# Kernel tuning notes

Hardware: AMD Instinct MI355X
Metric: run time of the kernel (lower is better)

Reference implementation:

```python
import jax, jax.numpy as jnp
import numpy as np

B, S, P, G, E = 16, 1024, 32, 64, 512
HD = E // 2          # head_dim = 256
SCALE = HD ** -0.5
LAMBDA_INIT = 0.8 - 0.6 * float(np.exp(-0.3 * 0.0))  # depth=0 -> 0.2
EPS = 1e-5


def setup_inputs() -> dict:
    key = jax.random.key(0)
    ks = jax.random.split(key, 12)
    inp = {
        'query': jax.random.normal(ks[0], (B, S, E), jnp.float32),
        'key': jax.random.normal(ks[1], (B, P, G, E), jnp.float32),
        'mask': jax.random.randint(ks[2], (B, S), 0, 2).astype(bool),
        'Wq': jax.random.normal(ks[3], (E, E), jnp.float32) * (E ** -0.5),
        'Wk': jax.random.normal(ks[4], (E, E), jnp.float32) * (E ** -0.5),
        'Wv': jax.random.normal(ks[5], (E, E), jnp.float32) * (E ** -0.5),
        'Wo': jax.random.normal(ks[6], (E, E), jnp.float32) * (E ** -0.5),
        'lq1': jax.random.normal(ks[7], (HD,), jnp.float32) * 0.1,
        'lk1': jax.random.normal(ks[8], (HD,), jnp.float32) * 0.1,
        'lq2': jax.random.normal(ks[9], (HD,), jnp.float32) * 0.1,
        'lk2': jax.random.normal(ks[10], (HD,), jnp.float32) * 0.1,
        'gamma': jnp.ones((E,), jnp.float32),
    }
    return inp


def reference(query, key, mask, Wq, Wk, Wv, Wo, lq1, lk1, lq2, lk2, gamma):
    b, s, e = query.shape
    _, p, g, _ = key.shape
    L = p * g
    key2d = key.reshape(b, L, e)

    Q = (query @ Wq).reshape(b, s, 2, HD).transpose(0, 2, 1, 3) * SCALE  # [B,2,S,hd]
    K = (key2d @ Wk).reshape(b, L, 2, HD).transpose(0, 2, 1, 3)          # [B,2,L,hd]
    V = key2d @ Wv                                                       # [B,L,E]

    scores = jnp.einsum('bhsd,bhld->bhsl', Q, K)                         # [B,2,S,L]
    # masked_fill(~mask, 0.0) with mask broadcast [B,1,S,1]
    scores = jnp.where(mask[:, None, :, None], scores, 0.0)
    attn = jax.nn.softmax(scores, axis=-1)

    lam1 = jnp.exp(jnp.sum(lq1 * lk1))
    lam2 = jnp.exp(jnp.sum(lq2 * lk2))
    lam = lam1 - lam2 + LAMBDA_INIT

    diff = attn[:, 0] - lam * attn[:, 1]                                 # [B,S,L]
    out2d = jnp.einsum('bsl,ble->bse', diff, V)                          # [B,S,E]

    # RMSNorm over last dim with affine gamma
    rms = out2d * jax.lax.rsqrt(jnp.mean(out2d * out2d, axis=-1, keepdims=True) + EPS)
    rms = rms * gamma
    out = (rms * (1.0 - LAMBDA_INIT)) @ Wo                               # [B,S,E]

    return out, diff.reshape(b, s, p, g)
```

## Files before the change

kernel.cpp:

```cpp
#include <hip/hip_runtime.h>
#include <hip/hip_bf16.h>


typedef short short8 __attribute__((ext_vector_type(8)));
typedef __bf16 bf16x8 __attribute__((ext_vector_type(8)));
typedef float f32x4 __attribute__((ext_vector_type(4)));

#define LDS_BYTES 16384
#define OUT0_ELEMS 8388608L

__global__ void probe_kernel(const void* gamma, const void* mask, int* flags)
{
    if (threadIdx.x == 0) {
        unsigned g = *(const unsigned*)gamma;
        flags[0] = (g == 0x3F800000u) ? 1 : 0;
        flags[1] = 0;
    }
    __syncthreads();
    const unsigned* mi = (const unsigned*)mask;
    int bad = 0;
    for (int i = threadIdx.x; i < 4096; i += blockDim.x)
        if (mi[i] > 1u) bad = 1;
    if (bad) atomicOr(&flags[1], 1);
}

__global__ void convert_mask(const void* __restrict__ mask, int* __restrict__ mi,
                             const int* __restrict__ flags)
{
    int i = blockIdx.x * 256 + threadIdx.x;
    if (flags[1]) mi[i] = ((const unsigned char*)mask)[i] ? 1 : 0;
    else          mi[i] = ((const int*)mask)[i] ? 1 : 0;
}

__device__ __forceinline__ float read_elem(const void* p, int i, int isf32)
{
    return isf32 ? ((const float*)p)[i]
                 : __bfloat162float(((const __hip_bfloat16*)p)[i]);
}

__global__ void convert_gamma(const void* __restrict__ gamma, float* __restrict__ g,
                              const int* __restrict__ flags)
{
    int i = blockIdx.x * 256 + threadIdx.x;
    g[i] = read_elem(gamma, i, flags[0]);
}

__global__ void transpose_w(const void* __restrict__ Wq, const void* __restrict__ Wk,
                            const void* __restrict__ Wv, const void* __restrict__ Wo,
                            __hip_bfloat16* __restrict__ dst, const int* __restrict__ flags)
{
    int which = blockIdx.y;
    const void* s = (which == 0) ? Wq : (which == 1) ? Wk : (which == 2) ? Wv : Wo;
    __hip_bfloat16* d = dst + (long)which * 262144;
    int idx = blockIdx.x * 256 + threadIdx.x;
    int k = idx >> 9, n = idx & 511;
    d[n * 512 + k] = __float2bfloat16(read_elem(s, idx, flags[0]));
}

__global__ void lam_kernel(const void* __restrict__ lq1, const void* __restrict__ lk1,
                           const void* __restrict__ lq2, const void* __restrict__ lk2,
                           float* __restrict__ lamp, const int* __restrict__ flags)
{
    int t = threadIdx.x;
    int f = flags[0];
    float s1 = 0.0f, s2 = 0.0f;
#pragma unroll
    for (int j = 0; j < 4; ++j) {
        int idx = t * 4 + j;
        s1 += read_elem(lq1, idx, f) * read_elem(lk1, idx, f);
        s2 += read_elem(lq2, idx, f) * read_elem(lk2, idx, f);
    }
#pragma unroll
    for (int off = 1; off < 64; off <<= 1) {
        s1 += __shfl_xor(s1, off);
        s2 += __shfl_xor(s2, off);
    }
    if (t == 0) *lamp = __expf(s1) - __expf(s2) + 0.2f;
}

__global__ void zero_lst(float* __restrict__ lst)
{
    lst[blockIdx.x * 256 + threadIdx.x] = 0.0f;
}

__device__ __forceinline__ void stage_u(const void* A, long aoff, int lda, int af32,
                                        const __hip_bfloat16* B, int ldb,
                                        int kt, char* smem, int tid)
{
    if (af32) {
#pragma unroll
        for (int j = 0; j < 2; ++j) {
            int chunk = j * 256 + tid;
            const float* g = (const float*)A + aoff + (long)(chunk >> 2) * lda + kt + (chunk & 3) * 8;
            f32x4 x0 = *(const f32x4*)g;
            f32x4 x1 = *(const f32x4*)(g + 4);
            __hip_bfloat16 tmp[8];
#pragma unroll
            for (int t = 0; t < 4; ++t) tmp[t] = __float2bfloat16(x0[t]);
#pragma unroll
            for (int t = 0; t < 4; ++t) tmp[4 + t] = __float2bfloat16(x1[t]);
            *(short8*)(smem + chunk * 16) = *(const short8*)tmp;
        }
    } else {
#pragma unroll
        for (int j = 0; j < 2; ++j) {
            int chunk = j * 256 + tid;
            const __hip_bfloat16* g = (const __hip_bfloat16*)A + aoff
                                    + (long)(chunk >> 2) * lda + kt + (chunk & 3) * 8;
            __builtin_amdgcn_global_load_lds(
                (__attribute__((address_space(1))) void*)g,
                (__attribute__((address_space(3))) void*)(smem + chunk * 16), 16, 0, 0);
        }
    }
#pragma unroll
    for (int j = 0; j < 2; ++j) {
        int chunk = j * 256 + tid;
        const __hip_bfloat16* g = B + (long)(chunk >> 2) * ldb + kt + (chunk & 3) * 8;
        __builtin_amdgcn_global_load_lds(
            (__attribute__((address_space(1))) void*)g,
            (__attribute__((address_space(3))) void*)(smem + 8192 + chunk * 16), 16, 0, 0);
    }
}

__device__ __forceinline__ void mfma_block(char* smem, int tid, f32x4 (&acc)[4][4])
{
    const int lane = tid & 63, wid = tid >> 6;
    const int wm = wid >> 1, wn = wid & 1;
    const int lm = lane & 15, lq = lane >> 4;
    short8 a[4], b[4];
#pragma unroll
    for (int i = 0; i < 4; ++i)
        a[i] = *(const short8*)(smem + (wm * 64 + i * 16 + lm) * 64 + lq * 16);
#pragma unroll
    for (int i = 0; i < 4; ++i)
        b[i] = *(const short8*)(smem + 8192 + (wn * 64 + i * 16 + lm) * 64 + lq * 16);
#pragma unroll
    for (int i = 0; i < 4; ++i)
#pragma unroll
        for (int j = 0; j < 4; ++j)
            acc[i][j] = __builtin_amdgcn_mfma_f32_16x16x32_bf16(
                __builtin_bit_cast(bf16x8, a[i]),
                __builtin_bit_cast(bf16x8, b[j]),
                acc[i][j], 0, 0, 0);
}

__device__ __forceinline__ void zero_acc(f32x4 (&acc)[4][4])
{
#pragma unroll
    for (int i = 0; i < 4; ++i)
#pragma unroll
        for (int j = 0; j < 4; ++j)
#pragma unroll
            for (int r = 0; r < 4; ++r) acc[i][j][r] = 0.0f;
}

__device__ __forceinline__ void tile_gemm_u(const void* A, long aoff, int lda, int af32,
                                            const __hip_bfloat16* B, int ldb, int K,
                                            char* smem, int tid, f32x4 (&acc)[4][4])
{
    zero_acc(acc);
    for (int kt = 0; kt < K; kt += 32) {
        __syncthreads();
        stage_u(A, aoff, lda, af32, B, ldb, kt, smem, tid);
        __syncthreads();
        mfma_block(smem, tid, acc);
    }
}

template <int MODE, int AF>
__launch_bounds__(256, 4)
__global__ void gemm_u(const void* __restrict__ A,
                       const __hip_bfloat16* __restrict__ B,
                       void* __restrict__ C,
                       int K, int lda, int ldb, int ldc,
                       long sA, long sB, long sC, float scale,
                       const int* __restrict__ flags)
{
    __shared__ __align__(16) char smem[LDS_BYTES];
    const int tid = threadIdx.x;
    const int bn = blockIdx.x, bm = blockIdx.y, bz = blockIdx.z;
    const int af32 = AF ? flags[0] : 0;
    const long aoff = (long)bz * sA + (long)bm * 128 * lda;
    const __hip_bfloat16* Bb = B + (long)bz * sB + (long)bn * 128 * ldb;

    f32x4 acc[4][4];
    tile_gemm_u(A, aoff, lda, af32, Bb, ldb, K, smem, tid, acc);

    const int f32o = (MODE == 3) ? flags[0] : 0;
    const int lane = tid & 63, wid = tid >> 6;
    const int wm = wid >> 1, wn = wid & 1;
    const int lm = lane & 15, lq = lane >> 4;
#pragma unroll
    for (int im = 0; im < 4; ++im)
#pragma unroll
        for (int in = 0; in < 4; ++in)
#pragma unroll
            for (int r = 0; r < 4; ++r) {
                int row = bm * 128 + wm * 64 + im * 16 + lq * 4 + r;
                int col = bn * 128 + wn * 64 + in * 16 + lm;
                float v = acc[im][in][r] * scale;
                if (MODE == 0) {
                    ((__hip_bfloat16*)C)[bz * sC + (long)row * ldc + col] = __float2bfloat16(v);
                } else if (MODE == 2) {
                    ((float*)C)[bz * sC + (long)row * ldc + col] = v;
                } else if (MODE == 3) {
                    long idx = bz * sC + (long)row * ldc + col;
                    if (f32o) ((float*)C)[idx] = v;
                    else      ((__hip_bfloat16*)C)[idx] = __float2bfloat16(v);
                } else {
                    int bb = row >> 11, l = row & 2047;
                    ((__hip_bfloat16*)C)[((long)bb * 512 + col) * 2048 + l] = __float2bfloat16(v);
                }
            }
}

__device__ __forceinline__ void score_epilogue(
    f32x4 (&acc)[4][4], char* smem, int tid,
    int nt, int st, int b, int bl, const int* __restrict__ mask,
    float* __restrict__ lstats, __hip_bfloat16* __restrict__ P, int h)
{
    const int lane = tid & 63, wid = tid >> 6;
    const int wm = wid >> 1, wn = wid & 1;
    const int lm = lane & 15, lq = lane >> 4;
    float esum[4][4];
#pragma unroll
    for (int im = 0; im < 4; ++im)
#pragma unroll
        for (int r = 0; r < 4; ++r) {
            int rl = wm * 64 + im * 16 + lq * 4 + r;
            int s  = st * 128 + rl;
            int mv = mask[b * 1024 + s];
            float es = 0.0f;
#pragma unroll
            for (int in = 0; in < 4; ++in) {
                int col = nt * 128 + wn * 64 + in * 16 + lm;
                float sc = mv ? acc[im][in][r] : 0.0f;
                float e  = __expf(sc);
                P[((long)bl * 1024 + s) * 2048 + col] = __float2bfloat16(e);
                float t = e;
                t += __shfl_xor(t, 1);
                t += __shfl_xor(t, 2);
                t += __shfl_xor(t, 4);
                t += __shfl_xor(t, 8);
                es += t;
            }
            esum[im][r] = es;
        }
    __syncthreads();
    float* red = (float*)smem;
    if (lm == 0) {
#pragma unroll
        for (int im = 0; im < 4; ++im)
#pragma unroll
            for (int r = 0; r < 4; ++r)
                red[wn * 128 + wm * 64 + im * 16 + lq * 4 + r] = esum[im][r];
    }
    __syncthreads();
    if (tid < 128)
        atomicAdd(&lstats[((long)(b * 2 + h)) * 1024 + st * 128 + tid],
                  red[tid] + red[128 + tid]);
}

__launch_bounds__(256, 3)
__global__ void score_kernel(const __hip_bfloat16* __restrict__ Q,
                             const __hip_bfloat16* __restrict__ Km,
                             const int* __restrict__ mask,
                             float* __restrict__ lstats,
                             __hip_bfloat16* __restrict__ P0,
                             __hip_bfloat16* __restrict__ P1,
                             int bbase)
{
    __shared__ __align__(16) char smem[LDS_BYTES];
    const int tid = threadIdx.x;
    const int nt = blockIdx.x, st = blockIdx.y, bl = blockIdx.z;
    const int b = bl + bbase;
    const long A0 = ((long)b * 1024 + st * 128) * 512;
    const __hip_bfloat16* B0 = Km + ((long)b * 2048 + nt * 128) * 512;

    f32x4 acc[4][4];
    tile_gemm_u(Q, A0, 512, 0, B0, 512, 256, smem, tid, acc);
    score_epilogue(acc, smem, tid, nt, st, b, bl, mask, lstats, P0, 0);
    tile_gemm_u(Q, A0 + 256, 512, 0, B0 + 256, 512, 256, smem, tid, acc);
    score_epilogue(acc, smem, tid, nt, st, b, bl, mask, lstats, P1, 1);
}

__global__ void finalize_kernel(__hip_bfloat16* P0,
                                const __hip_bfloat16* __restrict__ P1,
                                const float* __restrict__ lstats,
                                const float* __restrict__ lamp,
                                void* dout, int bbase,
                                const int* __restrict__ flags)
{
    const long row = blockIdx.x;
    const int bl = (int)(row >> 10), s = (int)(row & 1023);
    const int b  = bl + bbase;
    const int tid = threadIdx.x;
    const float lam = *lamp;
    const float i0 = 1.0f / lstats[((long)(b * 2)) * 1024 + s];
    const float i1 = lam  / lstats[((long)(b * 2 + 1)) * 1024 + s];
    const long lbase = row * 2048 + (long)tid * 8;

    union { short8 v; __hip_bfloat16 h[8]; } u0, u1, ub;
    u0.v = *(const short8*)(P0 + lbase);
    u1.v = *(const short8*)(P1 + lbase);
    float d[8];
#pragma unroll
    for (int j = 0; j < 8; ++j)
        d[j] = __bfloat162float(u0.h[j]) * i0 - __bfloat162float(u1.h[j]) * i1;

    const long gidx = ((long)b * 1024 + s) * 2048 + (long)tid * 8;
    if (flags[0]) {
        float* outF = (float*)dout + OUT0_ELEMS;
        f32x4 v0, v1;
#pragma unroll
        for (int j = 0; j < 4; ++j) { v0[j] = d[j]; v1[j] = d[4 + j]; }
        *(f32x4*)(outF + gidx)     = v0;
        *(f32x4*)(outF + gidx + 4) = v1;
    } else {
        __hip_bfloat16* outH = (__hip_bfloat16*)dout + OUT0_ELEMS;
        union { short8 v; __hip_bfloat16 h[8]; } uo;
#pragma unroll
        for (int j = 0; j < 8; ++j) uo.h[j] = __float2bfloat16(d[j]);
        *(short8*)(outH + gidx) = uo.v;
    }
#pragma unroll
    for (int j = 0; j < 8; ++j) ub.h[j] = __float2bfloat16(d[j]);
    *(short8*)(P0 + lbase) = ub.v;
}

__global__ void rmsnorm_kernel(const float* __restrict__ X,
                               const float* __restrict__ gamma,
                               __hip_bfloat16* __restrict__ Y)
{
    long row = blockIdx.x;
    int lane = threadIdx.x;
    const float* x = X + row * 512 + lane * 8;
    f32x4 v0 = *(const f32x4*)x;
    f32x4 v1 = *(const f32x4*)(x + 4);
    float ss = v0[0] * v0[0] + v0[1] * v0[1] + v0[2] * v0[2] + v0[3] * v0[3]
             + v1[0] * v1[0] + v1[1] * v1[1] + v1[2] * v1[2] + v1[3] * v1[3];
#pragma unroll
    for (int off = 1; off < 64; off <<= 1) ss += __shfl_xor(ss, off);
    float rinv = rsqrtf(ss * (1.0f / 512.0f) + 1e-5f) * 0.8f;
#pragma unroll
    for (int j = 0; j < 4; ++j)
        Y[row * 512 + lane * 8 + j] = __float2bfloat16(v0[j] * rinv * gamma[lane * 8 + j]);
#pragma unroll
    for (int j = 0; j < 4; ++j)
        Y[row * 512 + lane * 8 + 4 + j] = __float2bfloat16(v1[j] * rinv * gamma[lane * 8 + 4 + j]);
}

extern "C" void kernel_launch(void* const* d_in, const int* in_sizes, int n_in,
                              void* d_out, int out_size, void* d_ws, size_t ws_size,
                              hipStream_t stream)
{
    const void* query = d_in[0];
    const void* key2d = d_in[1];
    const void* maskp = d_in[2];
    const void* Wq    = d_in[3];
    const void* Wk    = d_in[4];
    const void* Wv    = d_in[5];
    const void* Wo    = d_in[6];
    const void* lq1   = d_in[7];
    const void* lk1   = d_in[8];
    const void* lq2   = d_in[9];
    const void* lk2   = d_in[10];
    const void* gamma = d_in[11];

    char* w = (char*)d_ws;
    __hip_bfloat16* WT    = (__hip_bfloat16*)(w);
    __hip_bfloat16* WqT   = WT;
    __hip_bfloat16* WkT   = WT + 262144;
    __hip_bfloat16* WvT   = WT + 524288;
    __hip_bfloat16* WoT   = WT + 786432;
    float*          lamp  = (float*)(w + 2097152);
    int*            flags = (int*)(w + 2097216);
    float*          gammaF= (float*)(w + 2097280);
    int*            maskI = (int*)(w + 2162688);
    __hip_bfloat16* Qb    = (__hip_bfloat16*)(w + 2228224);
    __hip_bfloat16* Kb    = (__hip_bfloat16*)(w + 19005440);
    __hip_bfloat16* Vt    = (__hip_bfloat16*)(w + 52559872);
    float*          lst   = (float*)(w + 86114304);
    float*          o2d   = (float*)(w + 86245376);
    __hip_bfloat16* rmsb  = (__hip_bfloat16*)(w + 119799808);
    __hip_bfloat16* diffBF= (__hip_bfloat16*)(w + 136577024);
    __hip_bfloat16* P1s   = (__hip_bfloat16*)(w + 103022592);

    const bool bigws = ws_size >= (136577024UL + 67108864UL);

    probe_kernel<<<1, 256, 0, stream>>>(gamma, maskp, flags);
    convert_mask<<<64, 256, 0, stream>>>(maskp, maskI, flags);
    convert_gamma<<<2, 256, 0, stream>>>(gamma, gammaF, flags);
    transpose_w<<<dim3(1024, 4, 1), 256, 0, stream>>>(Wq, Wk, Wv, Wo, WT, flags);
    lam_kernel<<<1, 64, 0, stream>>>(lq1, lk1, lq2, lk2, lamp, flags);
    zero_lst<<<128, 256, 0, stream>>>(lst);

    gemm_u<0, 1><<<dim3(4, 128, 1), 256, 0, stream>>>(query, WqT, Qb,
        512, 512, 512, 512, 0, 0, 0, 0.0625f, flags);
    gemm_u<0, 1><<<dim3(4, 256, 1), 256, 0, stream>>>(key2d, WkT, Kb,
        512, 512, 512, 512, 0, 0, 0, 1.0f, flags);
    gemm_u<1, 1><<<dim3(4, 256, 1), 256, 0, stream>>>(key2d, WvT, Vt,
        512, 512, 512, 0, 0, 0, 0, 1.0f, flags);

    if (bigws) {
        for (int h = 0; h < 2; ++h) {
            int bb = h * 8;
            __hip_bfloat16* P0 = diffBF + (long)bb * 1024 * 2048;
            score_kernel<<<dim3(16, 8, 8), 256, 0, stream>>>(Qb, Kb, maskI, lst,
                P0, P1s, bb);
            finalize_kernel<<<8192, 256, 0, stream>>>(P0, P1s, lst, lamp,
                d_out, bb, flags);
        }
        gemm_u<2, 0><<<dim3(4, 8, 16), 256, 0, stream>>>(diffBF, Vt, o2d,
            2048, 2048, 2048, 512, 1024L * 2048, 512L * 2048, 1024L * 512, 1.0f, flags);
    } else {
        __hip_bfloat16* scratch = (__hip_bfloat16*)d_out;
        for (int h = 0; h < 2; ++h) {
            int bb = h * 8;
            score_kernel<<<dim3(16, 8, 8), 256, 0, stream>>>(Qb, Kb, maskI, lst,
                scratch, P1s, bb);
            finalize_kernel<<<8192, 256, 0, stream>>>(scratch, P1s, lst, lamp,
                d_out, bb, flags);
            gemm_u<2, 0><<<dim3(4, 8, 8), 256, 0, stream>>>(scratch,
                Vt + (long)bb * 512 * 2048, o2d + (long)bb * 1024 * 512,
                2048, 2048, 2048, 512, 1024L * 2048, 512L * 2048, 1024L * 512, 1.0f, flags);
        }
    }

    rmsnorm_kernel<<<16384, 64, 0, stream>>>(o2d, gammaF, rmsb);

    gemm_u<3, 0><<<dim3(4, 128, 1), 256, 0, stream>>>(rmsb, WoT, d_out,
        512, 512, 512, 512, 0, 0, 1024L * 512, 1.0f, flags);
}
```

Measured before the change: 646.0 us.

## Fuse softmax normalization and diff computation into the diff@V GEMM

Adds a dv_fused kernel that reads the unnormalized score probabilities P0/P1, applies the per-row softmax normalizers and lambda to form diff on the fly, stages it in LDS, and runs the MFMA GEMM against V. The blocks with bn==0 also write diff to the output. This removes the separate finalize kernel and the write and re-read of the diff matrix. With a large enough workspace, all 16 batches are also handled in a single score launch. In exchange, the A operand is now loaded synchronously with conversion arithmetic and no async prefetch, and P0/P1 are read four times, once per column block.

After: 672.1 us. +4.0%, slower.

```diff
diff --git a/kernel.cpp b/kernel.cpp
--- a/kernel.cpp
+++ b/kernel.cpp
@@ -282,6 +282,97 @@
     score_epilogue(acc, smem, tid, nt, st, b, bl, mask, lstats, P0, 0);
     tile_gemm_u(Q, A0 + 256, 512, 0, B0 + 256, 512, 256, smem, tid, acc);
     score_epilogue(acc, smem, tid, nt, st, b, bl, mask, lstats, P1, 1);
+}
+
+__launch_bounds__(256, 3)
+__global__ void dv_fused(const __hip_bfloat16* __restrict__ P0,
+                         const __hip_bfloat16* __restrict__ P1,
+                         const __hip_bfloat16* __restrict__ Vt,
+                         const float* __restrict__ lst,
+                         const float* __restrict__ lamp,
+                         float* __restrict__ o2d,
+                         void* __restrict__ dout,
+                         int bbase, const int* __restrict__ flags)
+{
+    __shared__ __align__(16) char smem[LDS_BYTES];
+    const int tid = threadIdx.x;
+    const int bn = blockIdx.x, bm = blockIdx.y, bz = blockIdx.z;
+    const int b = bz + bbase;
+    const float lam = *lamp;
+
+    int srow[2]; float i0[2], i1[2];
+#pragma unroll
+    for (int j = 0; j < 2; ++j) {
+        srow[j] = bm * 128 + j * 64 + (tid >> 2);
+        i0[j] = 1.0f / lst[((long)(b * 2)) * 1024 + srow[j]];
+        i1[j] = lam  / lst[((long)(b * 2 + 1)) * 1024 + srow[j]];
+    }
+
+    const __hip_bfloat16* Bb = Vt + (long)b * (512L * 2048) + (long)bn * 128 * 2048;
+    const int f32o = flags[0];
+    float* doutF = (float*)dout + OUT0_ELEMS;
+    __hip_bfloat16* doutH = (__hip_bfloat16*)dout + OUT0_ELEMS;
+
+    f32x4 acc[4][4];
+    zero_acc(acc);
+
+    for (int kt = 0; kt < 2048; kt += 32) {
+        __syncthreads();
+#pragma unroll
+        for (int j = 0; j < 2; ++j) {
+            int chunk = j * 256 + tid;
+            int kc = kt + (chunk & 3) * 8;
+            long off = ((long)bz * 1024 + srow[j]) * 2048 + kc;
+            union { short8 v; __hip_bfloat16 h[8]; } u0, u1;
+            u0.v = *(const short8*)(P0 + off);
+            u1.v = *(const short8*)(P1 + off);
+            float d[8];
+#pragma unroll
+            for (int t = 0; t < 8; ++t)
+                d[t] = __bfloat162float(u0.h[t]) * i0[j]
+                     - __bfloat162float(u1.h[t]) * i1[j];
+            __hip_bfloat16 tmp[8];
+#pragma unroll
+            for (int t = 0; t < 8; ++t) tmp[t] = __float2bfloat16(d[t]);
+            *(short8*)(smem + chunk * 16) = *(const short8*)tmp;
+            if (bn == 0) {
+                long g = ((long)b * 1024 + srow[j]) * 2048 + kc;
+                if (f32o) {
+                    f32x4 v0, v1;
+#pragma unroll
+                    for (int t = 0; t < 4; ++t) { v0[t] = d[t]; v1[t] = d[4 + t]; }
+                    *(f32x4*)(doutF + g)     = v0;
+                    *(f32x4*)(doutF + g + 4) = v1;
+                } else {
+                    *(short8*)(doutH + g) = *(const short8*)tmp;
+                }
+            }
+        }
+#pragma unroll
+        for (int j = 0; j < 2; ++j) {
+            int chunk = j * 256 + tid;
+            const __hip_bfloat16* g = Bb + (long)(chunk >> 2) * 2048 + kt + (chunk & 3) * 8;
+            __builtin_amdgcn_global_load_lds(
+                (__attribute__((address_space(1))) void*)g,
+                (__attribute__((address_space(3))) void*)(smem + 8192 + chunk * 16), 16, 0, 0);
+        }
+        __syncthreads();
+        mfma_block(smem, tid, acc);
+    }
+
+    const int lane = tid & 63, wid = tid >> 6;
+    const int wm = wid >> 1, wn = wid & 1;
+    const int lm = lane & 15, lq = lane >> 4;
+#pragma unroll
+    for (int im = 0; im < 4; ++im)
+#pragma unroll
+        for (int in = 0; in < 4; ++in)
+#pragma unroll
+            for (int r = 0; r < 4; ++r) {
+                int row = bm * 128 + wm * 64 + im * 16 + lq * 4 + r;
+                int col = bn * 128 + wn * 64 + in * 16 + lm;
+                o2d[((long)b * 1024 + row) * 512 + col] = acc[im][in][r];
+            }
 }
 
 __global__ void finalize_kernel(__hip_bfloat16* P0,
@@ -386,7 +477,8 @@
     __hip_bfloat16* diffBF= (__hip_bfloat16*)(w + 136577024);
     __hip_bfloat16* P1s   = (__hip_bfloat16*)(w + 103022592);
 
-    const bool bigws = ws_size >= (136577024UL + 67108864UL);
+    const bool hugews = ws_size >= 270794752UL;
+    const bool bigws  = ws_size >= 203685888UL;
 
     probe_kernel<<<1, 256, 0, stream>>>(gamma, maskp, flags);
     convert_mask<<<64, 256, 0, stream>>>(maskp, maskI, flags);
@@ -402,17 +494,23 @@
     gemm_u<1, 1><<<dim3(4, 256, 1), 256, 0, stream>>>(key2d, WvT, Vt,
         512, 512, 512, 0, 0, 0, 0, 1.0f, flags);
 
-    if (bigws) {
+    if (hugews) {
+        __hip_bfloat16* P0f = diffBF;
+        __hip_bfloat16* P1f = diffBF + 33554432L;
+        score_kernel<<<dim3(16, 8, 16), 256, 0, stream>>>(Qb, Kb, maskI, lst,
+            P0f, P1f, 0);
+        dv_fused<<<dim3(4, 8, 16), 256, 0, stream>>>(P0f, P1f, Vt, lst, lamp,
+            o2d, d_out, 0, flags);
+    } else if (bigws) {
+        __hip_bfloat16* P0h = diffBF;
+        __hip_bfloat16* P1h = diffBF + 16777216L;
         for (int h = 0; h < 2; ++h) {
             int bb = h * 8;
-            __hip_bfloat16* P0 = diffBF + (long)bb * 1024 * 2048;
             score_kernel<<<dim3(16, 8, 8), 256, 0, stream>>>(Qb, Kb, maskI, lst,
-                P0, P1s, bb);
-            finalize_kernel<<<8192, 256, 0, stream>>>(P0, P1s, lst, lamp,
-                d_out, bb, flags);
-        }
-        gemm_u<2, 0><<<dim3(4, 8, 16), 256, 0, stream>>>(diffBF, Vt, o2d,
-            2048, 2048, 2048, 512, 1024L * 2048, 512L * 2048, 1024L * 512, 1.0f, flags);
+                P0h, P1h, bb);
+            dv_fused<<<dim3(4, 8, 8), 256, 0, stream>>>(P0h, P1h, Vt, lst, lamp,
+                o2d, d_out, bb, flags);
+        }
     } else {
         __hip_bfloat16* scratch = (__hip_bfloat16*)d_out;
         for (int h = 0; h < 2; ++h) {
```
